# Optimization experiments

Hardware: AMD Instinct MI355X
Metric: run time of the kernel (lower is better)

The kernel has to match this reference:

```python
import jax, jax.numpy as jnp
import numpy as np


def setup_inputs() -> dict:
    key = jax.random.key(0)
    ks = jax.random.split(key, 12)
    N, D = 150000, 100          # user_num + news_num nodes, emb_dim
    T, E, S = 16, 262144, 4096  # timesteps, edges/step, seeds/step
    CAT, K = 20, 9
    return {
        "node_emb": jax.random.normal(ks[0], (N, D), jnp.float32),
        "cx": jax.random.normal(ks[1], (N, D), jnp.float32),
        "rel_emb": jax.random.normal(ks[2], (CAT, D), jnp.float32),
        "W_ih": jax.random.normal(ks[3], (4 * D, D), jnp.float32) * 0.1,
        "W_hh": jax.random.normal(ks[4], (4 * D, D), jnp.float32) * 0.1,
        "b_ih": jax.random.normal(ks[5], (4 * D,), jnp.float32) * 0.1,
        "b_hh": jax.random.normal(ks[6], (4 * D,), jnp.float32) * 0.1,
        "src": jax.random.randint(ks[7], (T, E), 0, N, jnp.int64),
        "dst": jax.random.randint(ks[8], (T, E), 0, N, jnp.int64),
        "cat": jax.random.randint(ks[9], (T, E), 0, CAT, jnp.int64),
        "seeds": jax.random.randint(ks[10], (T, S), 0, 100000, jnp.int64),
        "cand_idx": jax.random.randint(ks[11], (T * S, K), 0, N, jnp.int64),
    }


def reference(node_emb, cx, rel_emb, W_ih, W_hh, b_ih, b_hh,
              src, dst, cat, seeds, cand_idx):
    N, D = node_emb.shape

    def step(carry, inputs):
        emb, c = carry
        s, d, ct, seed = inputs
        # previous hidden/cell state of seed users (before aggregation)
        h_prev = emb[seed]            # [S, D]
        c_prev = c[seed]              # [S, D]
        # edge-weighted gather-multiply-mean aggregation (send_and_recv)
        msg = emb[s] * rel_emb[ct]    # [E, D]
        agg = jax.ops.segment_sum(msg, d, num_segments=N)          # [N, D]
        cnt = jax.ops.segment_sum(jnp.ones(d.shape, emb.dtype), d,
                                  num_segments=N)                  # [N]
        emb = emb + agg / jnp.maximum(cnt, 1.0)[:, None]           # residual add
        # LSTMCell update on seed users
        x = emb[seed]                                              # [S, D]
        gates = x @ W_ih.T + b_ih + h_prev @ W_hh.T + b_hh         # [S, 4D]
        i_g, f_g, g_g, o_g = jnp.split(gates, 4, axis=-1)
        c_new = jax.nn.sigmoid(f_g) * c_prev + jax.nn.sigmoid(i_g) * jnp.tanh(g_g)
        h_new = jax.nn.sigmoid(o_g) * jnp.tanh(c_new)
        emb = emb.at[seed].set(h_new)
        c = c.at[seed].set(c_new)
        return (emb, c), h_new

    (emb_final, _), seed_embs = jax.lax.scan(
        step, (node_emb, cx), (src, dst, cat, seeds))
    # seed_embs: [T, S, D] -> per-click user embeddings
    user = seed_embs.reshape(-1, D)           # [T*S, D]
    cand = emb_final[cand_idx]                # [T*S, K, D]
    scores = jnp.einsum('nd,nkd->nk', user, cand)
    return scores
```

## Files before the change

kernel.cpp:

```cpp
#include <hip/hip_runtime.h>
#include <math.h>

#define N_NODES 150000
#define NODE_STRIDE 150016
#define DIM 100
#define D4 25
#define T_STEPS 16
#define E_EDGES 262144
#define S_SEEDS 4096
#define K_CAND 9
#define SPB 16

#define CB 64
#define BSPAN 2344
#define EPT 8
#define EPB (256 * EPT)
#define CBLK (E_EDGES / EPB)

__device__ __forceinline__ float sigmoidf_(float x) {
    return 1.0f / (1.0f + __expf(-x));
}


__global__ __launch_bounds__(256) void coarse_hist(
    const int* __restrict__ dst, int* __restrict__ bh) {
    int t = blockIdx.x / CBLK;
    int blk = blockIdx.x % CBLK;
    int base = t * E_EDGES + blk * EPB;
    int tid = threadIdx.x;
    __shared__ int h[CB];
    if (tid < CB) h[tid] = 0;
    __syncthreads();
#pragma unroll
    for (int e = 0; e < EPT; e++) {
        int d = dst[base + e * 256 + tid];
        atomicAdd(&h[d / BSPAN], 1);
    }
    __syncthreads();
    if (tid < CB) bh[(t * CBLK + blk) * CB + tid] = h[tid];
}

__global__ __launch_bounds__(64) void scan_bh(
    int* __restrict__ bh, int* __restrict__ coffs) {
    int t = blockIdx.x;
    int b = threadIdx.x;
    int run = 0;
    for (int blk = 0; blk < CBLK; blk++) {
        int idx = (t * CBLK + blk) * CB + b;
        int v = bh[idx];
        bh[idx] = run;
        run += v;
    }
    __shared__ int tot[CB];
    tot[b] = run;
    __syncthreads();
    if (b == 0) {
        int r = 0;
        for (int i = 0; i < CB; i++) { int c = tot[i]; tot[i] = r; r += c; }
    }
    __syncthreads();
    coffs[t * (CB + 1) + b] = tot[b];
    if (b == 0) coffs[t * (CB + 1) + CB] = E_EDGES;
}

__global__ __launch_bounds__(256) void coarse_scatter(
    const int* __restrict__ src, const int* __restrict__ dst,
    const int* __restrict__ cat, const int* __restrict__ bh,
    const int* __restrict__ coffs, int2* __restrict__ cbuf) {
    int t = blockIdx.x / CBLK;
    int blk = blockIdx.x % CBLK;
    int base = t * E_EDGES + blk * EPB;
    int tid = threadIdx.x;
    __shared__ int h[CB];
    __shared__ int gbase[CB];
    if (tid < CB) h[tid] = 0;
    __syncthreads();
    int rank[EPT], bb[EPT], dd[EPT];
#pragma unroll
    for (int e = 0; e < EPT; e++) {
        int d = dst[base + e * 256 + tid];
        int b = d / BSPAN;
        dd[e] = d; bb[e] = b;
        rank[e] = atomicAdd(&h[b], 1);
    }
    __syncthreads();
    if (tid < CB)
        gbase[tid] = coffs[t * (CB + 1) + tid] + bh[(t * CBLK + blk) * CB + tid];
    __syncthreads();
#pragma unroll
    for (int e = 0; e < EPT; e++) {
        int i = base + e * 256 + tid;
        int2 en;
        en.x = src[i] | (cat[i] << 18);
        en.y = dd[e];
        cbuf[(size_t)t * E_EDGES + gbase[bb[e]] + rank[e]] = en;
    }
}

__global__ __launch_bounds__(256) void fine_build(
    const int2* __restrict__ cbuf, const int* __restrict__ coffs,
    int4* __restrict__ meta, int* __restrict__ sorted) {
    int t = blockIdx.x >> 6;
    int b = blockIdx.x & 63;
    int node0 = b * BSPAN;
    int nodes = min(BSPAN, N_NODES - node0);
    int ebeg = coffs[t * (CB + 1) + b];
    int eend = coffs[t * (CB + 1) + b + 1];
    const int2* ebuf = cbuf + (size_t)t * E_EDGES;
    int4* mt = meta + (size_t)t * NODE_STRIDE;
    int* srt = sorted + (size_t)t * E_EDGES;
    __shared__ int cnt[BSPAN];
    __shared__ int begs[BSPAN];
    __shared__ int sums[256];
    int tid = threadIdx.x;

    for (int j = tid; j < BSPAN; j += 256) cnt[j] = 0;
    __syncthreads();
    for (int e = ebeg + tid; e < eend; e += 256)
        atomicAdd(&cnt[ebuf[e].y - node0], 1);
    __syncthreads();

    const int chunk = (BSPAN + 255) / 256;
    int cbeg = tid * chunk;
    int cend = min(cbeg + chunk, BSPAN);
    int s = 0;
    for (int j = cbeg; j < cend; j++) s += cnt[j];
    sums[tid] = s;
    __syncthreads();
    for (int d = 1; d < 256; d <<= 1) {
        int v = (tid >= d) ? sums[tid - d] : 0;
        __syncthreads();
        sums[tid] += v;
        __syncthreads();
    }
    int run = (tid == 0) ? 0 : sums[tid - 1];
    for (int j = cbeg; j < cend; j++) {
        int c = cnt[j];
        begs[j] = run;
        cnt[j] = run;
        run += c;
    }
    __syncthreads();

    for (int e = ebeg + tid; e < eend; e += 256) {
        int2 en = ebuf[e];
        int pos = atomicAdd(&cnt[en.y - node0], 1);
        srt[ebeg + pos] = en.x;
    }
    __syncthreads();

    for (int j = tid; j < nodes; j += 256) {
        int lbeg = begs[j];
        int deg = cnt[j] - lbeg;
        int gbeg = ebeg + lbeg;
        int4 m;
        m.x = gbeg | (deg << 19);
        m.y = (deg > 0) ? srt[gbeg] : 0;
        m.z = (deg > 1) ? srt[gbeg + 1] : 0;
        m.w = (deg > 2) ? srt[gbeg + 2] : 0;
        mt[node0 + j] = m;
    }
}

__global__ __launch_bounds__(256) void fused_agg(
    const float* __restrict__ emb_in, float* __restrict__ emb_out,
    const float* __restrict__ rel_emb, const int4* __restrict__ meta,
    const int* __restrict__ sorted) {
    unsigned idx = blockIdx.x * 256u + threadIdx.x;
    unsigned node = idx / 25u;
    unsigned q = idx - node * 25u;
    if (node >= N_NODES) return;
    float4 own = ((const float4*)(emb_in + (size_t)node * DIM))[q];
    int4 m = meta[node];
    int deg = ((unsigned)m.x) >> 19;
    int beg = m.x & 0x7FFFF;
    float4 acc = make_float4(0.f, 0.f, 0.f, 0.f);
    if (deg > 0) {
        float4 mm = ((const float4*)(emb_in + (size_t)(m.y & 0x3FFFF) * DIM))[q];
        float4 rr = ((const float4*)(rel_emb + (size_t)(m.y >> 18) * DIM))[q];
        acc.x += mm.x * rr.x; acc.y += mm.y * rr.y;
        acc.z += mm.z * rr.z; acc.w += mm.w * rr.w;
    }
    if (deg > 1) {
        float4 mm = ((const float4*)(emb_in + (size_t)(m.z & 0x3FFFF) * DIM))[q];
        float4 rr = ((const float4*)(rel_emb + (size_t)(m.z >> 18) * DIM))[q];
        acc.x += mm.x * rr.x; acc.y += mm.y * rr.y;
        acc.z += mm.z * rr.z; acc.w += mm.w * rr.w;
    }
    if (deg > 2) {
        float4 mm = ((const float4*)(emb_in + (size_t)(m.w & 0x3FFFF) * DIM))[q];
        float4 rr = ((const float4*)(rel_emb + (size_t)(m.w >> 18) * DIM))[q];
        acc.x += mm.x * rr.x; acc.y += mm.y * rr.y;
        acc.z += mm.z * rr.z; acc.w += mm.w * rr.w;
    }
    for (int e = beg + 3; e < beg + deg; e++) {
        int p = sorted[e];
        float4 mm = ((const float4*)(emb_in + (size_t)(p & 0x3FFFF) * DIM))[q];
        float4 rr = ((const float4*)(rel_emb + (size_t)(p >> 18) * DIM))[q];
        acc.x += mm.x * rr.x; acc.y += mm.y * rr.y;
        acc.z += mm.z * rr.z; acc.w += mm.w * rr.w;
    }
    float inv = (deg > 0) ? 1.0f / (float)deg : 0.0f;
    own.x += acc.x * inv; own.y += acc.y * inv;
    own.z += acc.z * inv; own.w += acc.w * inv;
    ((float4*)(emb_out + (size_t)node * DIM))[q] = own;
}

__global__ __launch_bounds__(512) void lstm_kernel(
    const float* __restrict__ emb_new, const float* __restrict__ emb_old,
    const float* __restrict__ c_state, const int* __restrict__ seeds,
    const float* __restrict__ W_ih, const float* __restrict__ W_hh,
    const float* __restrict__ b_ih, const float* __restrict__ b_hh,
    float* __restrict__ h_out, float* __restrict__ c_out) {
    __shared__ __align__(16) float xs[SPB][DIM];
    __shared__ __align__(16) float hs[SPB][DIM];
    __shared__ __align__(16) float gates[SPB][4 * DIM];
    int tid = threadIdx.x;
    int base = blockIdx.x * SPB;

    for (int idx = tid; idx < SPB * D4; idx += 512) {
        int s = idx / D4, q = idx - s * D4;
        int node = seeds[base + s];
        ((float4*)xs[s])[q] = ((const float4*)(emb_new + (size_t)node * DIM))[q];
        ((float4*)hs[s])[q] = ((const float4*)(emb_old + (size_t)node * DIM))[q];
    }
    __syncthreads();

    if (tid < 4 * DIM) {
        int j = tid;
        float acc[SPB];
#pragma unroll
        for (int s = 0; s < SPB; s++) acc[s] = 0.0f;
        const float4* wi = (const float4*)(W_ih + (size_t)j * DIM);
        const float4* wh = (const float4*)(W_hh + (size_t)j * DIM);
        for (int dc = 0; dc < D4; dc++) {
            float4 a = wi[dc], b = wh[dc];
#pragma unroll
            for (int s = 0; s < SPB; s++) {
                float4 x = ((const float4*)xs[s])[dc];
                float4 h = ((const float4*)hs[s])[dc];
                acc[s] += x.x * a.x + x.y * a.y + x.z * a.z + x.w * a.w
                        + h.x * b.x + h.y * b.y + h.z * b.z + h.w * b.w;
            }
        }
        float bb = b_ih[j] + b_hh[j];
#pragma unroll
        for (int s = 0; s < SPB; s++) gates[s][j] = acc[s] + bb;
    }
    __syncthreads();

    for (int idx = tid; idx < SPB * D4; idx += 512) {
        int s = idx / D4, q = idx - s * D4;
        int node = seeds[base + s];
        float4 ig = ((const float4*)gates[s])[q];
        float4 fg = ((const float4*)(gates[s] + DIM))[q];
        float4 gg = ((const float4*)(gates[s] + 2 * DIM))[q];
        float4 og = ((const float4*)(gates[s] + 3 * DIM))[q];
        float4 cp = ((const float4*)(c_state + (size_t)node * DIM))[q];
        float4 cn, hn;
        cn.x = sigmoidf_(fg.x) * cp.x + sigmoidf_(ig.x) * tanhf(gg.x);
        cn.y = sigmoidf_(fg.y) * cp.y + sigmoidf_(ig.y) * tanhf(gg.y);
        cn.z = sigmoidf_(fg.z) * cp.z + sigmoidf_(ig.z) * tanhf(gg.z);
        cn.w = sigmoidf_(fg.w) * cp.w + sigmoidf_(ig.w) * tanhf(gg.w);
        hn.x = sigmoidf_(og.x) * tanhf(cn.x);
        hn.y = sigmoidf_(og.y) * tanhf(cn.y);
        hn.z = sigmoidf_(og.z) * tanhf(cn.z);
        hn.w = sigmoidf_(og.w) * tanhf(cn.w);
        ((float4*)(h_out + (size_t)(base + s) * DIM))[q] = hn;
        ((float4*)(c_out + (size_t)(base + s) * DIM))[q] = cn;
    }
}

__global__ __launch_bounds__(256) void scatter_seed(
    float* __restrict__ emb, float* __restrict__ c_state,
    const int* __restrict__ seeds,
    const float* __restrict__ h_new, const float* __restrict__ c_new) {
    int i = blockIdx.x * blockDim.x + threadIdx.x;
    int sd = i / D4, q = i - sd * D4;
    int node = seeds[sd];
    ((float4*)(emb + (size_t)node * DIM))[q] =
        ((const float4*)(h_new + (size_t)sd * DIM))[q];
    ((float4*)(c_state + (size_t)node * DIM))[q] =
        ((const float4*)(c_new + (size_t)sd * DIM))[q];
}

__global__ __launch_bounds__(64) void score_kernel(
    const float* __restrict__ seed_h, const float* __restrict__ emb,
    const int* __restrict__ cand_idx, float* __restrict__ out) {
    int n = blockIdx.x;
    int lane = threadIdx.x;
    bool hi = lane + 64 < DIM;
    float u0 = seed_h[(size_t)n * DIM + lane];
    float u1 = hi ? seed_h[(size_t)n * DIM + lane + 64] : 0.0f;
    int cd[K_CAND];
#pragma unroll
    for (int k = 0; k < K_CAND; k++) cd[k] = cand_idx[n * K_CAND + k];
    float p[K_CAND];
#pragma unroll
    for (int k = 0; k < K_CAND; k++) {
        const float* ce = emb + (size_t)cd[k] * DIM;
        p[k] = u0 * ce[lane];
        if (hi) p[k] += u1 * ce[lane + 64];
    }
#pragma unroll
    for (int k = 0; k < K_CAND; k++) {
        for (int off = 32; off > 0; off >>= 1)
            p[k] += __shfl_down(p[k], off);
        if (lane == 0) out[n * K_CAND + k] = p[k];
    }
}

extern "C" void kernel_launch(void* const* d_in, const int* in_sizes, int n_in,
                              void* d_out, int out_size, void* d_ws, size_t ws_size,
                              hipStream_t stream) {
    const float* node_emb = (const float*)d_in[0];
    const float* cx       = (const float*)d_in[1];
    const float* rel_emb  = (const float*)d_in[2];
    const float* W_ih     = (const float*)d_in[3];
    const float* W_hh     = (const float*)d_in[4];
    const float* b_ih     = (const float*)d_in[5];
    const float* b_hh     = (const float*)d_in[6];
    const int*   src      = (const int*)d_in[7];
    const int*   dst      = (const int*)d_in[8];
    const int*   cat      = (const int*)d_in[9];
    const int*   seeds    = (const int*)d_in[10];
    const int*   cand     = (const int*)d_in[11];
    float* out = (float*)d_out;

    char* wsb = (char*)d_ws;
    float* emb_a = (float*)wsb; wsb += sizeof(float) * (size_t)N_NODES * DIM;
    float* emb_b = (float*)wsb; wsb += sizeof(float) * (size_t)N_NODES * DIM;
    float* cst   = (float*)wsb; wsb += sizeof(float) * (size_t)N_NODES * DIM;
    float* cnew  = (float*)wsb; wsb += sizeof(float) * (size_t)S_SEEDS * DIM;
    float* seedh = (float*)wsb; wsb += sizeof(float) * (size_t)T_STEPS * S_SEEDS * DIM;
    int4* meta   = (int4*)wsb; wsb += sizeof(int4) * (size_t)T_STEPS * NODE_STRIDE;
    int* sorted  = (int*)wsb; wsb += sizeof(int) * (size_t)T_STEPS * E_EDGES;
    int* bh      = (int*)wsb; wsb += sizeof(int) * (size_t)T_STEPS * CBLK * CB;
    int* coffs   = (int*)wsb; wsb += sizeof(int) * T_STEPS * (CB + 1);
    int2* cbuf = (int2*)emb_b;

    coarse_hist<<<T_STEPS * CBLK, 256, 0, stream>>>(dst, bh);
    scan_bh<<<T_STEPS, 64, 0, stream>>>(bh, coffs);
    coarse_scatter<<<T_STEPS * CBLK, 256, 0, stream>>>(
        src, dst, cat, bh, coffs, cbuf);
    fine_build<<<T_STEPS * CB, 256, 0, stream>>>(cbuf, coffs, meta, sorted);

    hipMemcpyAsync(cst, cx, sizeof(float) * (size_t)N_NODES * DIM,
                   hipMemcpyDeviceToDevice, stream);

    const float* cur = node_emb;
    float* bufs[2] = {emb_b, emb_a};
    const int agg_blocks = (N_NODES * D4 + 255) / 256;
    for (int t = 0; t < T_STEPS; t++) {
        float* nxt = bufs[t & 1];
        fused_agg<<<agg_blocks, 256, 0, stream>>>(
            cur, nxt, rel_emb,
            meta + (size_t)t * NODE_STRIDE, sorted + (size_t)t * E_EDGES);
        lstm_kernel<<<S_SEEDS / SPB, 512, 0, stream>>>(
            nxt, cur, cst, seeds + (size_t)t * S_SEEDS,
            W_ih, W_hh, b_ih, b_hh,
            seedh + (size_t)t * S_SEEDS * DIM, cnew);
        scatter_seed<<<(S_SEEDS * D4) / 256, 256, 0, stream>>>(
            nxt, cst, seeds + (size_t)t * S_SEEDS,
            seedh + (size_t)t * S_SEEDS * DIM, cnew);
        cur = nxt;
    }
    score_kernel<<<T_STEPS * S_SEEDS, 64, 0, stream>>>(seedh, cur, cand, out);
}
```

Measured before the change: 1.517 ms.

## Merge aggregation and LSTM into one role-split kernel per timestep

The separate aggregation and LSTM kernels become one launch. The first blocks recompute the aggregated values for their seed rows directly from the current embeddings and run the LSTM, while the remaining blocks do the full-graph aggregation into the next buffer. This removes one kernel launch and the serial dependency between the two stages, so the LSTM no longer waits for the whole aggregation to finish. The cost is redundant aggregation work for seed rows, and the combined kernel uses a larger 512-thread block with the LSTM's shared-memory footprint, which may reduce occupancy for the aggregation role.

Measured after the change: 1.482 ms. -2.3%, faster.

```diff
diff --git a/kernel.cpp b/kernel.cpp
--- a/kernel.cpp
+++ b/kernel.cpp
@@ -10,6 +10,7 @@
 #define S_SEEDS 4096
 #define K_CAND 9
 #define SPB 16
+#define LSTM_BLOCKS (S_SEEDS / SPB)
 
 #define CB 64
 #define BSPAN 2344
@@ -162,14 +163,10 @@
     }
 }
 
-__global__ __launch_bounds__(256) void fused_agg(
-    const float* __restrict__ emb_in, float* __restrict__ emb_out,
-    const float* __restrict__ rel_emb, const int4* __restrict__ meta,
-    const int* __restrict__ sorted) {
-    unsigned idx = blockIdx.x * 256u + threadIdx.x;
-    unsigned node = idx / 25u;
-    unsigned q = idx - node * 25u;
-    if (node >= N_NODES) return;
+__device__ __forceinline__ float4 agg_val(
+    const float* __restrict__ emb_in, const float* __restrict__ rel_emb,
+    const int4* __restrict__ meta, const int* __restrict__ sorted,
+    int node, int q) {
     float4 own = ((const float4*)(emb_in + (size_t)node * DIM))[q];
     int4 m = meta[node];
     int deg = ((unsigned)m.x) >> 19;
@@ -203,12 +200,14 @@
     float inv = (deg > 0) ? 1.0f / (float)deg : 0.0f;
     own.x += acc.x * inv; own.y += acc.y * inv;
     own.z += acc.z * inv; own.w += acc.w * inv;
-    ((float4*)(emb_out + (size_t)node * DIM))[q] = own;
-}
-
-__global__ __launch_bounds__(512) void lstm_kernel(
-    const float* __restrict__ emb_new, const float* __restrict__ emb_old,
-    const float* __restrict__ c_state, const int* __restrict__ seeds,
+    return own;
+}
+
+__global__ __launch_bounds__(512, 8) void agg_lstm(
+    const float* __restrict__ cur, float* __restrict__ nxt,
+    const float* __restrict__ rel_emb, const int4* __restrict__ meta,
+    const int* __restrict__ sorted, const float* __restrict__ c_state,
+    const int* __restrict__ seeds,
     const float* __restrict__ W_ih, const float* __restrict__ W_hh,
     const float* __restrict__ b_ih, const float* __restrict__ b_hh,
     float* __restrict__ h_out, float* __restrict__ c_out) {
@@ -216,58 +215,68 @@
     __shared__ __align__(16) float hs[SPB][DIM];
     __shared__ __align__(16) float gates[SPB][4 * DIM];
     int tid = threadIdx.x;
-    int base = blockIdx.x * SPB;
-
-    for (int idx = tid; idx < SPB * D4; idx += 512) {
-        int s = idx / D4, q = idx - s * D4;
-        int node = seeds[base + s];
-        ((float4*)xs[s])[q] = ((const float4*)(emb_new + (size_t)node * DIM))[q];
-        ((float4*)hs[s])[q] = ((const float4*)(emb_old + (size_t)node * DIM))[q];
-    }
-    __syncthreads();
-
-    if (tid < 4 * DIM) {
-        int j = tid;
-        float acc[SPB];
-#pragma unroll
-        for (int s = 0; s < SPB; s++) acc[s] = 0.0f;
-        const float4* wi = (const float4*)(W_ih + (size_t)j * DIM);
-        const float4* wh = (const float4*)(W_hh + (size_t)j * DIM);
-        for (int dc = 0; dc < D4; dc++) {
-            float4 a = wi[dc], b = wh[dc];
-#pragma unroll
-            for (int s = 0; s < SPB; s++) {
-                float4 x = ((const float4*)xs[s])[dc];
-                float4 h = ((const float4*)hs[s])[dc];
-                acc[s] += x.x * a.x + x.y * a.y + x.z * a.z + x.w * a.w
-                        + h.x * b.x + h.y * b.y + h.z * b.z + h.w * b.w;
+
+    if (blockIdx.x < LSTM_BLOCKS) {
+        int base = blockIdx.x * SPB;
+        for (int idx = tid; idx < SPB * D4; idx += 512) {
+            int s = idx / D4, q = idx - s * D4;
+            int node = seeds[base + s];
+            ((float4*)xs[s])[q] = agg_val(cur, rel_emb, meta, sorted, node, q);
+            ((float4*)hs[s])[q] = ((const float4*)(cur + (size_t)node * DIM))[q];
+        }
+        __syncthreads();
+
+        if (tid < 4 * DIM) {
+            int j = tid;
+            float acc[SPB];
+#pragma unroll
+            for (int s = 0; s < SPB; s++) acc[s] = 0.0f;
+            const float4* wi = (const float4*)(W_ih + (size_t)j * DIM);
+            const float4* wh = (const float4*)(W_hh + (size_t)j * DIM);
+            for (int dc = 0; dc < D4; dc++) {
+                float4 a = wi[dc], b = wh[dc];
+#pragma unroll
+                for (int s = 0; s < SPB; s++) {
+                    float4 x = ((const float4*)xs[s])[dc];
+                    float4 h = ((const float4*)hs[s])[dc];
+                    acc[s] += x.x * a.x + x.y * a.y + x.z * a.z + x.w * a.w
+                            + h.x * b.x + h.y * b.y + h.z * b.z + h.w * b.w;
+                }
             }
+            float bb = b_ih[j] + b_hh[j];
+#pragma unroll
+            for (int s = 0; s < SPB; s++) gates[s][j] = acc[s] + bb;
         }
-        float bb = b_ih[j] + b_hh[j];
-#pragma unroll
-        for (int s = 0; s < SPB; s++) gates[s][j] = acc[s] + bb;
-    }
-    __syncthreads();
-
-    for (int idx = tid; idx < SPB * D4; idx += 512) {
-        int s = idx / D4, q = idx - s * D4;
-        int node = seeds[base + s];
-        float4 ig = ((const float4*)gates[s])[q];
-        float4 fg = ((const float4*)(gates[s] + DIM))[q];
-        float4 gg = ((const float4*)(gates[s] + 2 * DIM))[q];
-        float4 og = ((const float4*)(gates[s] + 3 * DIM))[q];
-        float4 cp = ((const float4*)(c_state + (size_t)node * DIM))[q];
-        float4 cn, hn;
-        cn.x = sigmoidf_(fg.x) * cp.x + sigmoidf_(ig.x) * tanhf(gg.x);
-        cn.y = sigmoidf_(fg.y) * cp.y + sigmoidf_(ig.y) * tanhf(gg.y);
-        cn.z = sigmoidf_(fg.z) * cp.z + sigmoidf_(ig.z) * tanhf(gg.z);
-        cn.w = sigmoidf_(fg.w) * cp.w + sigmoidf_(ig.w) * tanhf(gg.w);
-        hn.x = sigmoidf_(og.x) * tanhf(cn.x);
-        hn.y = sigmoidf_(og.y) * tanhf(cn.y);
-        hn.z = sigmoidf_(og.z) * tanhf(cn.z);
-        hn.w = sigmoidf_(og.w) * tanhf(cn.w);
-        ((float4*)(h_out + (size_t)(base + s) * DIM))[q] = hn;
-        ((float4*)(c_out + (size_t)(base + s) * DIM))[q] = cn;
+        __syncthreads();
+
+        for (int idx = tid; idx < SPB * D4; idx += 512) {
+            int s = idx / D4, q = idx - s * D4;
+            int node = seeds[base + s];
+            float4 ig = ((const float4*)gates[s])[q];
+            float4 fg = ((const float4*)(gates[s] + DIM))[q];
+            float4 gg = ((const float4*)(gates[s] + 2 * DIM))[q];
+            float4 og = ((const float4*)(gates[s] + 3 * DIM))[q];
+            float4 cp = ((const float4*)(c_state + (size_t)node * DIM))[q];
+            float4 cn, hn;
+            cn.x = sigmoidf_(fg.x) * cp.x + sigmoidf_(ig.x) * tanhf(gg.x);
+            cn.y = sigmoidf_(fg.y) * cp.y + sigmoidf_(ig.y) * tanhf(gg.y);
+            cn.z = sigmoidf_(fg.z) * cp.z + sigmoidf_(ig.z) * tanhf(gg.z);
+            cn.w = sigmoidf_(fg.w) * cp.w + sigmoidf_(ig.w) * tanhf(gg.w);
+            hn.x = sigmoidf_(og.x) * tanhf(cn.x);
+            hn.y = sigmoidf_(og.y) * tanhf(cn.y);
+            hn.z = sigmoidf_(og.z) * tanhf(cn.z);
+            hn.w = sigmoidf_(og.w) * tanhf(cn.w);
+            ((float4*)(h_out + (size_t)(base + s) * DIM))[q] = hn;
+            ((float4*)(c_out + (size_t)(base + s) * DIM))[q] = cn;
+        }
+    } else {
+        unsigned idx = (blockIdx.x - LSTM_BLOCKS) * 512u + tid;
+        unsigned node = idx / 25u;
+        unsigned q = idx - node * 25u;
+        if (node < N_NODES) {
+            float4 v = agg_val(cur, rel_emb, meta, sorted, (int)node, (int)q);
+            ((float4*)(nxt + (size_t)node * DIM))[q] = v;
+        }
     }
 }
 
@@ -350,14 +359,13 @@
 
     const float* cur = node_emb;
     float* bufs[2] = {emb_b, emb_a};
-    const int agg_blocks = (N_NODES * D4 + 255) / 256;
+    const int agg_role_blocks = (N_NODES * D4 + 511) / 512;
     for (int t = 0; t < T_STEPS; t++) {
         float* nxt = bufs[t & 1];
-        fused_agg<<<agg_blocks, 256, 0, stream>>>(
+        agg_lstm<<<LSTM_BLOCKS + agg_role_blocks, 512, 0, stream>>>(
             cur, nxt, rel_emb,
-            meta + (size_t)t * NODE_STRIDE, sorted + (size_t)t * E_EDGES);
-        lstm_kernel<<<S_SEEDS / SPB, 512, 0, stream>>>(
-            nxt, cur, cst, seeds + (size_t)t * S_SEEDS,
+            meta + (size_t)t * NODE_STRIDE, sorted + (size_t)t * E_EDGES,
+            cst, seeds + (size_t)t * S_SEEDS,
             W_ih, W_hh, b_ih, b_hh,
             seedh + (size_t)t * S_SEEDS * DIM, cnew);
         scatter_seed<<<(S_SEEDS * D4) / 256, 256, 0, stream>>>(
```
